# Optimization experiments

Measured on AMD Instinct MI355X. Metric: run time of the kernel, lower is better.

Reference implementation:

```python
import jax, jax.numpy as jnp
import numpy as np

B, S, D = 2, 2048, 512   # batch, seq_len, input_dim
H, E = 8, 512            # num_heads, per-head output_dim (full D per head, per source)
NEG = -1e9


def setup_inputs() -> dict:
    key = jax.random.key(0)
    ks = jax.random.split(key, 12)
    sc = 1.0 / np.sqrt(D)
    inp = {
        "query": jax.random.normal(ks[0], (B, S, D), jnp.float32),
        "key":   jax.random.normal(ks[1], (B, S, D), jnp.float32),
        "value": jax.random.normal(ks[2], (B, S, D), jnp.float32),
        "mask":  jax.random.randint(ks[3], (B, S, S), 0, 2).astype(bool),
        # stacked per-head Linear weights: [H, D, E] (x @ W layout)
        "Wq": jax.random.normal(ks[4], (H, D, E), jnp.float32) * sc,
        "bq": jax.random.normal(ks[5], (H, E), jnp.float32) * 0.02,
        "Wk": jax.random.normal(ks[6], (H, D, E), jnp.float32) * sc,
        "bk": jax.random.normal(ks[7], (H, E), jnp.float32) * 0.02,
        "Wv": jax.random.normal(ks[8], (H, D, E), jnp.float32) * sc,
        "bv": jax.random.normal(ks[9], (H, E), jnp.float32) * 0.02,
        # output projection: Linear(H*E, E)
        "Wo": jax.random.normal(ks[10], (H * E, E), jnp.float32) * (1.0 / np.sqrt(H * E)),
        "bo": jax.random.normal(ks[11], (E,), jnp.float32) * 0.02,
    }
    return inp


def reference(query, key, value, mask, Wq, bq, Wk, bk, Wv, bv, Wo, bo):
    # Batched per-head projections (replaces the Python per-head loop)
    q = jnp.einsum("bsd,hde->bhse", query, Wq) + bq[None, :, None, :]
    k = jnp.einsum("bsd,hde->bhse", key,   Wk) + bk[None, :, None, :]
    v = jnp.einsum("bsd,hde->bhse", value, Wv) + bv[None, :, None, :]
    # NOTE: source has NO 1/sqrt(d) scaling — kept faithful.
    scores = jnp.einsum("bhse,bhte->bhst", q, k)           # [B,H,S,S]
    scores = jnp.where(mask[:, None, :, :], scores, NEG)    # masked_fill(mask==0, -1e9)
    attn = jax.nn.softmax(scores, axis=-1)
    out = jnp.einsum("bhst,bhte->bhse", attn, v)            # [B,H,S,E]
    # concat heads along last dim in head order -> [B,S,H*E]
    cat = out.transpose(0, 2, 1, 3).reshape(out.shape[0], out.shape[2], -1)
    return cat @ Wo + bo
```

## Files before the change

### kernel.cpp

```cpp
#include <hip/hip_runtime.h>

#define B_  2
#define S_  2048
#define D_  512
#define H_  8
#define E_  512
#define HE_ 4096

typedef _Float16 half8_t  __attribute__((ext_vector_type(8)));
typedef _Float16 half4_t  __attribute__((ext_vector_type(4)));
typedef float    floatx4  __attribute__((ext_vector_type(4)));
typedef __attribute__((address_space(1))) const unsigned int* gas_ptr;
typedef __attribute__((address_space(3))) unsigned int*       las_ptr;

__global__ __launch_bounds__(256) void cast3_f16_kernel(
    const float* __restrict__ s0, const float* __restrict__ s1, const float* __restrict__ s2,
    _Float16* __restrict__ d0, _Float16* __restrict__ d1, _Float16* __restrict__ d2, int n4) {
    int i = blockIdx.x * 256 + threadIdx.x;
    if (i >= n4) return;
    const float* s = (blockIdx.y == 0) ? s0 : (blockIdx.y == 1) ? s1 : s2;
    _Float16*    d = (blockIdx.y == 0) ? d0 : (blockIdx.y == 1) ? d1 : d2;
    float4 v = ((const float4*)s)[i];
    half4_t h = { (_Float16)v.x, (_Float16)v.y, (_Float16)v.z, (_Float16)v.w };
    ((half4_t*)d)[i] = h;
}

__global__ __launch_bounds__(256) void transpose3_cast_kernel(
    const float* __restrict__ p0, const float* __restrict__ p1, const float* __restrict__ p2,
    _Float16* __restrict__ q0, _Float16* __restrict__ q1, _Float16* __restrict__ q2,
    int R, int C) {
    __shared__ float t[32][33];
    int which = blockIdx.z >> 3, hh = blockIdx.z & 7;
    const float* src = ((which == 0) ? p0 : (which == 1) ? p1 : p2) + (long long)hh * R * C;
    _Float16*    dst = ((which == 0) ? q0 : (which == 1) ? q1 : q2) + (long long)hh * R * C;
    int c0 = blockIdx.x * 32, r0 = blockIdx.y * 32;
    int tx = threadIdx.x, ty = threadIdx.y;
#pragma unroll
    for (int i = 0; i < 32; i += 8)
        t[ty + i][tx] = src[(long long)(r0 + ty + i) * C + (c0 + tx)];
    __syncthreads();
#pragma unroll
    for (int i = 0; i < 32; i += 8)
        dst[(long long)(c0 + ty + i) * R + (r0 + tx)] = (_Float16)t[tx][ty + i];
}

__global__ __launch_bounds__(256) void transpose_cast_kernel(const float* __restrict__ src,
                                                             _Float16* __restrict__ dst,
                                                             int R, int C) {
    __shared__ float t[32][33];
    int c0 = blockIdx.x * 32, r0 = blockIdx.y * 32;
    int tx = threadIdx.x, ty = threadIdx.y;
#pragma unroll
    for (int i = 0; i < 32; i += 8)
        t[ty + i][tx] = src[(long long)(r0 + ty + i) * C + (c0 + tx)];
    __syncthreads();
#pragma unroll
    for (int i = 0; i < 32; i += 8)
        dst[(long long)(c0 + ty + i) * R + (r0 + tx)] = (_Float16)t[tx][ty + i];
}


__device__ __forceinline__ void xcd_decode(int& z, int& by, int& bx) {
    int gx = gridDim.x, gy = gridDim.y, gz = gridDim.z;
    int bpz = gx * gy;
    int fid = blockIdx.x + gx * (blockIdx.y + gy * blockIdx.z);
    if ((gz & 7) == 0) {
        int xcd = fid & 7, sl = fid >> 3;
        int zg = gz >> 3;
        z = xcd * zg + sl / bpz;
        int inner = sl % bpz;
        by = inner / gx;
        bx = inner % gx;
    } else {
        z = blockIdx.z; by = blockIdx.y; bx = blockIdx.x;
    }
}

__global__ __launch_bounds__(256) void gemm_qkv_kernel(
    const _Float16* __restrict__ Xq, const _Float16* __restrict__ Xk, const _Float16* __restrict__ Xv,
    const _Float16* __restrict__ WqT, const _Float16* __restrict__ WkT, const _Float16* __restrict__ WvT,
    const float* __restrict__ bq, const float* __restrict__ bk, const float* __restrict__ bv,
    _Float16* __restrict__ Qb, _Float16* __restrict__ Kb, _Float16* __restrict__ VT)
{
    int z, byy, bxx;
    xcd_decode(z, byy, bxx);
    int which = z >> 4, zz = z & 15;
    int bb = zz >> 3, hh = zz & 7;
    const _Float16* A  = ((which == 0) ? Xq : (which == 1) ? Xk : Xv) + (long long)bb * S_ * D_;
    const _Float16* Bt = ((which == 0) ? WqT : (which == 1) ? WkT : WvT) + (long long)hh * E_ * D_;
    const float* bias  = ((which == 0) ? bq : (which == 1) ? bk : bv) + hh * E_;

    int m0 = byy * 128;
    int n0 = bxx * 128;

    __shared__ __align__(16) _Float16 As[2][128][32];
    __shared__ __align__(16) _Float16 Bs[2][128][32];

    int tid  = threadIdx.x;
    int wave = tid >> 6, lane = tid & 63;
    int quad = lane >> 4, l16 = lane & 15;
    int wy = (wave >> 1) * 64, wx = (wave & 1) * 64;
    int pw = wave & 1, rw = (wave >> 1) * 64;
    int sr = lane >> 2;
    int scg = ((lane & 3) ^ ((lane >> 3) & 3)) * 8;
    _Float16* lA0 = &As[pw][rw][0];
    _Float16* lB0 = &Bs[pw][rw][0];
    int cra = (quad ^ ((l16 >> 1) & 3)) * 8;

    floatx4 acc[4][4] = {};

    for (int k0 = 0; k0 < D_; k0 += 64) {
        if (k0) __syncthreads();
        const _Float16* gA = A + (long long)(m0 + rw + sr) * D_ + k0 + pw * 32 + scg;
        const _Float16* gB = Bt + (long long)(n0 + rw + sr) * D_ + k0 + pw * 32 + scg;
#pragma unroll
        for (int j = 0; j < 4; j++) {
            __builtin_amdgcn_global_load_lds((gas_ptr)(gA + (long long)(j * 16) * D_),
                                             (las_ptr)(lA0 + j * 512), 16, 0, 0);
            __builtin_amdgcn_global_load_lds((gas_ptr)(gB + (long long)(j * 16) * D_),
                                             (las_ptr)(lB0 + j * 512), 16, 0, 0);
        }
        __syncthreads();
#pragma unroll
        for (int kc = 0; kc < 2; kc++) {
            half8_t af[4], bf[4];
#pragma unroll
            for (int i = 0; i < 4; i++) {
                af[i] = *(const half8_t*)&As[kc][wy + i * 16 + l16][cra];
                bf[i] = *(const half8_t*)&Bs[kc][wx + i * 16 + l16][cra];
            }
#pragma unroll
            for (int mi = 0; mi < 4; mi++)
#pragma unroll
                for (int ni = 0; ni < 4; ni++)
                    acc[mi][ni] = __builtin_amdgcn_mfma_f32_16x16x32_f16(af[mi], bf[ni], acc[mi][ni], 0, 0, 0);
        }
    }

    if (which < 2) {
        _Float16* C = ((which == 0) ? Qb : Kb) + ((long long)(bb * H_ + hh)) * S_ * E_;
#pragma unroll
        for (int mi = 0; mi < 4; mi++)
#pragma unroll
            for (int ni = 0; ni < 4; ni++)
#pragma unroll
                for (int r = 0; r < 4; r++) {
                    int row = m0 + wy + mi * 16 + quad * 4 + r;
                    int col = n0 + wx + ni * 16 + l16;
                    C[(long long)row * E_ + col] = (_Float16)(acc[mi][ni][r] + bias[col]);
                }
    } else {
        _Float16* C = VT + ((long long)(bb * H_ + hh)) * E_ * S_;
#pragma unroll
        for (int mi = 0; mi < 4; mi++)
#pragma unroll
            for (int ni = 0; ni < 4; ni++) {
                int row = m0 + wy + mi * 16 + quad * 4;
                int col = n0 + wx + ni * 16 + l16;
                float bcol = bias[col];
                half4_t h4 = { (_Float16)(acc[mi][ni][0] + bcol), (_Float16)(acc[mi][ni][1] + bcol),
                               (_Float16)(acc[mi][ni][2] + bcol), (_Float16)(acc[mi][ni][3] + bcol) };
                *(half4_t*)(C + (long long)col * S_ + row) = h4;
            }
    }
}

__global__ __launch_bounds__(512, 2) void gemm_bt256_kernel(
    const _Float16* __restrict__ A, const _Float16* __restrict__ Bt,
    _Float16* __restrict__ C,
    int K, int lda, int ldb,
    long long a_z, long long b_z, long long c_b, long long c_h, int c_rs, int hdiv)
{
    int z, byy, bxx;
    xcd_decode(z, byy, bxx);
    int bb = z / hdiv, hh = z % hdiv;
    A  += (long long)z * a_z;
    Bt += (long long)z * b_z;
    _Float16* Cz = C + bb * c_b + hh * c_h;

    int m0 = byy * 256;
    int n0 = bxx * 256;

    __shared__ __align__(16) _Float16 As[4][256][32];
    __shared__ __align__(16) _Float16 Bs[4][256][32];

    int tid  = threadIdx.x;
    int wave = tid >> 6, lane = tid & 63;
    int quad = lane >> 4, l16 = lane & 15;
    int wm128 = (wave >> 2) * 128;
    int wn64  = (wave & 3) * 64;
    int wave16 = wave * 16;
    int sr = lane >> 2;
    int scg = ((lane & 3) ^ ((lane >> 3) & 3)) * 8;
    int cra = (quad ^ ((l16 >> 1) & 3)) * 8;

    auto STAGE = [&](int t) {
        int buf = t & 3;
        int kk = t << 5;
        const _Float16* gA = A + (long long)(m0 + wave16 + sr) * lda + kk + scg;
        const _Float16* gB = Bt + (long long)(n0 + wave16 + sr) * ldb + kk + scg;
        _Float16* lA = &As[buf][wave16][0];
        _Float16* lB = &Bs[buf][wave16][0];
#pragma unroll
        for (int j = 0; j < 2; j++) {
            __builtin_amdgcn_global_load_lds((gas_ptr)(gA + (long long)(j * 128) * lda),
                                             (las_ptr)(lA + j * 128 * 32), 16, 0, 0);
            __builtin_amdgcn_global_load_lds((gas_ptr)(gB + (long long)(j * 128) * ldb),
                                             (las_ptr)(lB + j * 128 * 32), 16, 0, 0);
        }
    };

    int nt = K >> 5;

    STAGE(0);
    if (nt > 1) STAGE(1);
    if (nt > 2) STAGE(2);
    if (nt > 2)      asm volatile("s_waitcnt vmcnt(8)" ::: "memory");
    else if (nt > 1) asm volatile("s_waitcnt vmcnt(4)" ::: "memory");
    else             asm volatile("s_waitcnt vmcnt(0)" ::: "memory");
    __builtin_amdgcn_s_barrier();

    floatx4 acc[8][4] = {};

    for (int t = 0; t < nt; ++t) {
        if (t + 3 < nt) STAGE(t + 3);
        int buf = t & 3;
        half8_t af[8], bf[4];
#pragma unroll
        for (int i = 0; i < 8; i++)
            af[i] = *(const half8_t*)&As[buf][wm128 + i * 16 + l16][cra];
#pragma unroll
        for (int i = 0; i < 4; i++)
            bf[i] = *(const half8_t*)&Bs[buf][wn64 + i * 16 + l16][cra];
#pragma unroll
        for (int mi = 0; mi < 8; mi++)
#pragma unroll
            for (int ni = 0; ni < 4; ni++)
                acc[mi][ni] = __builtin_amdgcn_mfma_f32_16x16x32_f16(af[mi], bf[ni], acc[mi][ni], 0, 0, 0);
        if (t + 1 < nt) {
            if (t + 3 < nt)      asm volatile("s_waitcnt vmcnt(8) lgkmcnt(0)" ::: "memory");
            else if (t + 2 < nt) asm volatile("s_waitcnt vmcnt(4) lgkmcnt(0)" ::: "memory");
            else                 asm volatile("s_waitcnt vmcnt(0) lgkmcnt(0)" ::: "memory");
            __builtin_amdgcn_s_barrier();
        }
    }

#pragma unroll
    for (int mi = 0; mi < 8; mi++)
#pragma unroll
        for (int ni = 0; ni < 4; ni++)
#pragma unroll
            for (int r = 0; r < 4; r++) {
                int row = m0 + wm128 + mi * 16 + quad * 4 + r;
                int col = n0 + wn64 + ni * 16 + l16;
                Cz[(long long)row * c_rs + col] = (_Float16)acc[mi][ni][r];
            }
}

__global__ __launch_bounds__(512) void softmax_mask8_kernel(_Float16* __restrict__ sc,
                                                            const int* __restrict__ mask)
{
    int b = blockIdx.z, s = blockIdx.x;
    int wave = threadIdx.x >> 6, lane = threadIdx.x & 63;
    _Float16* row = sc + ((long long)(b * H_ + wave) * S_ + s) * S_;
    const int* mrow = mask + ((long long)b * S_ + s) * S_;

    half8_t h[4];
    float v[32];
    float mx = -3.0e38f;
#pragma unroll
    for (int j = 0; j < 4; j++) {
        int c = j * 512 + lane * 8;
        h[j] = *(const half8_t*)(row + c);
        int4 mA = *(const int4*)(mrow + c);
        int4 mB = *(const int4*)(mrow + c + 4);
        int mm[8] = { mA.x, mA.y, mA.z, mA.w, mB.x, mB.y, mB.z, mB.w };
#pragma unroll
        for (int e = 0; e < 8; e++) {
            float val = mm[e] ? (float)h[j][e] : -1.0e9f;
            v[j * 8 + e] = val;
            mx = fmaxf(mx, val);
        }
    }
#pragma unroll
    for (int o = 32; o > 0; o >>= 1) mx = fmaxf(mx, __shfl_xor(mx, o));

    float sum = 0.0f;
#pragma unroll
    for (int i = 0; i < 32; i++) { v[i] = __expf(v[i] - mx); sum += v[i]; }
#pragma unroll
    for (int o = 32; o > 0; o >>= 1) sum += __shfl_xor(sum, o);

    float inv = 1.0f / sum;
#pragma unroll
    for (int j = 0; j < 4; j++) {
#pragma unroll
        for (int e = 0; e < 8; e++) h[j][e] = (_Float16)(v[j * 8 + e] * inv);
        *(half8_t*)(row + j * 512 + lane * 8) = h[j];
    }
}

__global__ __launch_bounds__(256) void gemm_bt_n64_splitk_kernel(
    const _Float16* __restrict__ A, const _Float16* __restrict__ Bt,
    const float* __restrict__ bias, float* __restrict__ C,
    int K, int lda, int ldb, int ldc, int ksplit)
{
    int m0 = blockIdx.y * 128;
    int n0 = blockIdx.x * 64;
    int kchunk = K / ksplit;
    int kbeg = blockIdx.z * kchunk;
    int kend = kbeg + kchunk;

    __shared__ __align__(16) _Float16 As[128][32];
    __shared__ __align__(16) _Float16 Bs[64][32];

    int tid  = threadIdx.x;
    int wave = tid >> 6, lane = tid & 63;
    int quad = lane >> 4, l16 = lane & 15;
    int wy = (wave >> 1) * 64, wx = (wave & 1) * 32;

    int srow = (wave << 4) + (lane >> 2);
    int scg = ((lane & 3) ^ ((lane >> 3) & 3)) * 8;
    _Float16* lA0 = &As[0][0] + (wave << 9);
    _Float16* lB0 = &Bs[0][0] + (wave << 9);
    int cra = (quad ^ ((l16 >> 1) & 3)) * 8;

    floatx4 acc[4][2] = {};

    for (int k0 = kbeg; k0 < kend; k0 += 32) {
        if (k0 != kbeg) __syncthreads();
        const _Float16* gA = A + (long long)(m0 + srow) * lda + k0 + scg;
        const _Float16* gB = Bt + (long long)(n0 + srow) * ldb + k0 + scg;
#pragma unroll
        for (int j = 0; j < 2; j++)
            __builtin_amdgcn_global_load_lds((gas_ptr)(gA + (long long)(j << 6) * lda),
                                             (las_ptr)(lA0 + (j << 11)), 16, 0, 0);
        __builtin_amdgcn_global_load_lds((gas_ptr)gB, (las_ptr)lB0, 16, 0, 0);
        __syncthreads();

        half8_t af[4], bf[2];
#pragma unroll
        for (int i = 0; i < 4; i++)
            af[i] = *(const half8_t*)&As[wy + i * 16 + l16][cra];
#pragma unroll
        for (int i = 0; i < 2; i++)
            bf[i] = *(const half8_t*)&Bs[wx + i * 16 + l16][cra];
#pragma unroll
        for (int mi = 0; mi < 4; mi++)
#pragma unroll
            for (int ni = 0; ni < 2; ni++)
                acc[mi][ni] = __builtin_amdgcn_mfma_f32_16x16x32_f16(af[mi], bf[ni], acc[mi][ni], 0, 0, 0);
    }

    int addb = (blockIdx.z == 0) && bias;
#pragma unroll
    for (int mi = 0; mi < 4; mi++)
#pragma unroll
        for (int ni = 0; ni < 2; ni++)
#pragma unroll
            for (int r = 0; r < 4; r++) {
                int row = m0 + wy + mi * 16 + quad * 4 + r;
                int col = n0 + wx + ni * 16 + l16;
                float v = acc[mi][ni][r];
                if (addb) v += bias[col];
                atomicAdd(&C[(long long)row * ldc + col], v);
            }
}

extern "C" void kernel_launch(void* const* d_in, const int* in_sizes, int n_in,
                              void* d_out, int out_size, void* d_ws, size_t ws_size,
                              hipStream_t stream)
{
    const float* qin = (const float*)d_in[0];
    const float* kin = (const float*)d_in[1];
    const float* vin = (const float*)d_in[2];
    const int*   mask = (const int*)d_in[3];
    const float* Wq = (const float*)d_in[4];
    const float* bq = (const float*)d_in[5];
    const float* Wk = (const float*)d_in[6];
    const float* bk = (const float*)d_in[7];
    const float* Wv = (const float*)d_in[8];
    const float* bv = (const float*)d_in[9];
    const float* Wo = (const float*)d_in[10];
    const float* bo = (const float*)d_in[11];
    float* out = (float*)d_out;

    char* ws = (char*)d_ws;
    size_t off = 0;
    _Float16* WoT = (_Float16*)(ws + off); off += (size_t)E_ * HE_ * 2;
    _Float16* Qb  = (_Float16*)(ws + off); off += (size_t)B_ * H_ * S_ * E_ * 2;
    _Float16* Kb  = (_Float16*)(ws + off); off += (size_t)B_ * H_ * S_ * E_ * 2;
    _Float16* VT  = (_Float16*)(ws + off); off += (size_t)B_ * H_ * E_ * S_ * 2;
    size_t region = off;
    _Float16* Xq  = (_Float16*)(ws + region);
    _Float16* Xk  = Xq  + (size_t)B_ * S_ * D_;
    _Float16* Xv  = Xk  + (size_t)B_ * S_ * D_;
    _Float16* WqT = Xv  + (size_t)B_ * S_ * D_;
    _Float16* WkT = WqT + (size_t)H_ * E_ * D_;
    _Float16* WvT = WkT + (size_t)H_ * E_ * D_;
    _Float16* SC  = (_Float16*)(ws + region);
    _Float16* cat = Qb;

    long long SE = (long long)S_ * E_;
    long long SS = (long long)S_ * S_;
    long long ES = (long long)E_ * S_;

    (void)hipMemsetAsync(d_out, 0, (size_t)out_size * sizeof(float), stream);

    int n4 = B_ * S_ * D_ / 4;
    cast3_f16_kernel<<<dim3(n4 / 256, 3), 256, 0, stream>>>(qin, kin, vin, Xq, Xk, Xv, n4);

    dim3 tb(32, 8);
    transpose3_cast_kernel<<<dim3(E_ / 32, D_ / 32, 24), tb, 0, stream>>>(
        Wq, Wk, Wv, WqT, WkT, WvT, D_, E_);
    transpose_cast_kernel<<<dim3(E_ / 32, HE_ / 32, 1), tb, 0, stream>>>(Wo, WoT, HE_, E_);

    gemm_qkv_kernel<<<dim3(E_ / 128, S_ / 128, 48), 256, 0, stream>>>(
        Xq, Xk, Xv, WqT, WkT, WvT, bq, bk, bv, Qb, Kb, VT);

    gemm_bt256_kernel<<<dim3(S_ / 256, S_ / 256, B_ * H_), 512, 0, stream>>>(
        Qb, Kb, SC, E_, E_, E_, SE, SE, 0, SS, S_, 32 );

    softmax_mask8_kernel<<<dim3(S_, 1, B_), 512, 0, stream>>>(SC, mask);

    gemm_bt256_kernel<<<dim3(E_ / 256, S_ / 256, B_ * H_), 512, 0, stream>>>(
        SC, VT, cat, S_, S_, S_, SS, ES, (long long)S_ * HE_, E_, HE_, H_);

    gemm_bt_n64_splitk_kernel<<<dim3(E_ / 64, (B_ * S_) / 128, 4), 256, 0, stream>>>(
        cat, WoT, bo, out, HE_, HE_, HE_, E_, 4);
}
```

Before: 533.3 us.

## Double-buffer LDS fragment reads in GEMM core and move QKV projection to 256 tiles

Factors the 256x256 GEMM main loop into a shared core that prefetches the next k-step's LDS fragments into a second register set while MFMAs run on the current one. MFMA sections get raised wave priority, and the barrier and waitcnt logic is restructured. The QKV projection moves from a 128x128 tile kernel onto this 256x256 core with 512 threads. The aim is to hide LDS read latency and raise per-block reuse, at the cost of more registers for the double fragments and fewer blocks in the QKV grid.

```diff
diff --git a/kernel.cpp b/kernel.cpp
--- a/kernel.cpp
+++ b/kernel.cpp
@@ -58,7 +58,6 @@
     for (int i = 0; i < 32; i += 8)
         dst[(long long)(c0 + ty + i) * R + (r0 + tx)] = (_Float16)t[tx][ty + i];
 }
-
 
 __device__ __forceinline__ void xcd_decode(int& z, int& by, int& bx) {
     int gx = gridDim.x, gy = gridDim.y, gz = gridDim.z;
@@ -76,114 +75,12 @@
     }
 }
 
-__global__ __launch_bounds__(256) void gemm_qkv_kernel(
-    const _Float16* __restrict__ Xq, const _Float16* __restrict__ Xk, const _Float16* __restrict__ Xv,
-    const _Float16* __restrict__ WqT, const _Float16* __restrict__ WkT, const _Float16* __restrict__ WvT,
-    const float* __restrict__ bq, const float* __restrict__ bk, const float* __restrict__ bv,
-    _Float16* __restrict__ Qb, _Float16* __restrict__ Kb, _Float16* __restrict__ VT)
-{
-    int z, byy, bxx;
-    xcd_decode(z, byy, bxx);
-    int which = z >> 4, zz = z & 15;
-    int bb = zz >> 3, hh = zz & 7;
-    const _Float16* A  = ((which == 0) ? Xq : (which == 1) ? Xk : Xv) + (long long)bb * S_ * D_;
-    const _Float16* Bt = ((which == 0) ? WqT : (which == 1) ? WkT : WvT) + (long long)hh * E_ * D_;
-    const float* bias  = ((which == 0) ? bq : (which == 1) ? bk : bv) + hh * E_;
-
-    int m0 = byy * 128;
-    int n0 = bxx * 128;
-
-    __shared__ __align__(16) _Float16 As[2][128][32];
-    __shared__ __align__(16) _Float16 Bs[2][128][32];
-
-    int tid  = threadIdx.x;
-    int wave = tid >> 6, lane = tid & 63;
-    int quad = lane >> 4, l16 = lane & 15;
-    int wy = (wave >> 1) * 64, wx = (wave & 1) * 64;
-    int pw = wave & 1, rw = (wave >> 1) * 64;
-    int sr = lane >> 2;
-    int scg = ((lane & 3) ^ ((lane >> 3) & 3)) * 8;
-    _Float16* lA0 = &As[pw][rw][0];
-    _Float16* lB0 = &Bs[pw][rw][0];
-    int cra = (quad ^ ((l16 >> 1) & 3)) * 8;
-
-    floatx4 acc[4][4] = {};
-
-    for (int k0 = 0; k0 < D_; k0 += 64) {
-        if (k0) __syncthreads();
-        const _Float16* gA = A + (long long)(m0 + rw + sr) * D_ + k0 + pw * 32 + scg;
-        const _Float16* gB = Bt + (long long)(n0 + rw + sr) * D_ + k0 + pw * 32 + scg;
-#pragma unroll
-        for (int j = 0; j < 4; j++) {
-            __builtin_amdgcn_global_load_lds((gas_ptr)(gA + (long long)(j * 16) * D_),
-                                             (las_ptr)(lA0 + j * 512), 16, 0, 0);
-            __builtin_amdgcn_global_load_lds((gas_ptr)(gB + (long long)(j * 16) * D_),
-                                             (las_ptr)(lB0 + j * 512), 16, 0, 0);
-        }
-        __syncthreads();
-#pragma unroll
-        for (int kc = 0; kc < 2; kc++) {
-            half8_t af[4], bf[4];
-#pragma unroll
-            for (int i = 0; i < 4; i++) {
-                af[i] = *(const half8_t*)&As[kc][wy + i * 16 + l16][cra];
-                bf[i] = *(const half8_t*)&Bs[kc][wx + i * 16 + l16][cra];
-            }
-#pragma unroll
-            for (int mi = 0; mi < 4; mi++)
-#pragma unroll
-                for (int ni = 0; ni < 4; ni++)
-                    acc[mi][ni] = __builtin_amdgcn_mfma_f32_16x16x32_f16(af[mi], bf[ni], acc[mi][ni], 0, 0, 0);
-        }
-    }
-
-    if (which < 2) {
-        _Float16* C = ((which == 0) ? Qb : Kb) + ((long long)(bb * H_ + hh)) * S_ * E_;
-#pragma unroll
-        for (int mi = 0; mi < 4; mi++)
-#pragma unroll
-            for (int ni = 0; ni < 4; ni++)
-#pragma unroll
-                for (int r = 0; r < 4; r++) {
-                    int row = m0 + wy + mi * 16 + quad * 4 + r;
-                    int col = n0 + wx + ni * 16 + l16;
-                    C[(long long)row * E_ + col] = (_Float16)(acc[mi][ni][r] + bias[col]);
-                }
-    } else {
-        _Float16* C = VT + ((long long)(bb * H_ + hh)) * E_ * S_;
-#pragma unroll
-        for (int mi = 0; mi < 4; mi++)
-#pragma unroll
-            for (int ni = 0; ni < 4; ni++) {
-                int row = m0 + wy + mi * 16 + quad * 4;
-                int col = n0 + wx + ni * 16 + l16;
-                float bcol = bias[col];
-                half4_t h4 = { (_Float16)(acc[mi][ni][0] + bcol), (_Float16)(acc[mi][ni][1] + bcol),
-                               (_Float16)(acc[mi][ni][2] + bcol), (_Float16)(acc[mi][ni][3] + bcol) };
-                *(half4_t*)(C + (long long)col * S_ + row) = h4;
-            }
-    }
-}
-
-__global__ __launch_bounds__(512, 2) void gemm_bt256_kernel(
+__device__ __forceinline__ void bt256_core(
     const _Float16* __restrict__ A, const _Float16* __restrict__ Bt,
-    _Float16* __restrict__ C,
-    int K, int lda, int ldb,
-    long long a_z, long long b_z, long long c_b, long long c_h, int c_rs, int hdiv)
-{
-    int z, byy, bxx;
-    xcd_decode(z, byy, bxx);
-    int bb = z / hdiv, hh = z % hdiv;
-    A  += (long long)z * a_z;
-    Bt += (long long)z * b_z;
-    _Float16* Cz = C + bb * c_b + hh * c_h;
-
-    int m0 = byy * 256;
-    int n0 = bxx * 256;
-
-    __shared__ __align__(16) _Float16 As[4][256][32];
-    __shared__ __align__(16) _Float16 Bs[4][256][32];
-
+    int lda, int ldb, int nt, int m0, int n0,
+    _Float16 (*As)[256][32], _Float16 (*Bs)[256][32],
+    floatx4 (&acc)[8][4])
+{
     int tid  = threadIdx.x;
     int wave = tid >> 6, lane = tid & 63;
     int quad = lane >> 4, l16 = lane & 15;
@@ -194,11 +91,13 @@
     int scg = ((lane & 3) ^ ((lane >> 3) & 3)) * 8;
     int cra = (quad ^ ((l16 >> 1) & 3)) * 8;
 
+    const _Float16* gA0 = A + (long long)(m0 + wave16 + sr) * lda + scg;
+    const _Float16* gB0 = Bt + (long long)(n0 + wave16 + sr) * ldb + scg;
+
     auto STAGE = [&](int t) {
         int buf = t & 3;
-        int kk = t << 5;
-        const _Float16* gA = A + (long long)(m0 + wave16 + sr) * lda + kk + scg;
-        const _Float16* gB = Bt + (long long)(n0 + wave16 + sr) * ldb + kk + scg;
+        const _Float16* gA = gA0 + (t << 5);
+        const _Float16* gB = gB0 + (t << 5);
         _Float16* lA = &As[buf][wave16][0];
         _Float16* lB = &Bs[buf][wave16][0];
 #pragma unroll
@@ -209,42 +108,85 @@
                                              (las_ptr)(lB + j * 128 * 32), 16, 0, 0);
         }
     };
-
-    int nt = K >> 5;
-
-    STAGE(0);
-    if (nt > 1) STAGE(1);
-    if (nt > 2) STAGE(2);
-    if (nt > 2)      asm volatile("s_waitcnt vmcnt(8)" ::: "memory");
-    else if (nt > 1) asm volatile("s_waitcnt vmcnt(4)" ::: "memory");
-    else             asm volatile("s_waitcnt vmcnt(0)" ::: "memory");
-    __builtin_amdgcn_s_barrier();
-
-    floatx4 acc[8][4] = {};
-
-    for (int t = 0; t < nt; ++t) {
-        if (t + 3 < nt) STAGE(t + 3);
+    auto DSREAD = [&](int t, half8_t (&fa)[8], half8_t (&fb)[4]) {
         int buf = t & 3;
-        half8_t af[8], bf[4];
 #pragma unroll
         for (int i = 0; i < 8; i++)
-            af[i] = *(const half8_t*)&As[buf][wm128 + i * 16 + l16][cra];
+            fa[i] = *(const half8_t*)&As[buf][wm128 + i * 16 + l16][cra];
 #pragma unroll
         for (int i = 0; i < 4; i++)
-            bf[i] = *(const half8_t*)&Bs[buf][wn64 + i * 16 + l16][cra];
+            fb[i] = *(const half8_t*)&Bs[buf][wn64 + i * 16 + l16][cra];
+    };
+    auto MFMA = [&](half8_t (&fa)[8], half8_t (&fb)[4]) {
+        __builtin_amdgcn_s_setprio(1);
 #pragma unroll
         for (int mi = 0; mi < 8; mi++)
 #pragma unroll
             for (int ni = 0; ni < 4; ni++)
-                acc[mi][ni] = __builtin_amdgcn_mfma_f32_16x16x32_f16(af[mi], bf[ni], acc[mi][ni], 0, 0, 0);
-        if (t + 1 < nt) {
-            if (t + 3 < nt)      asm volatile("s_waitcnt vmcnt(8) lgkmcnt(0)" ::: "memory");
-            else if (t + 2 < nt) asm volatile("s_waitcnt vmcnt(4) lgkmcnt(0)" ::: "memory");
-            else                 asm volatile("s_waitcnt vmcnt(0) lgkmcnt(0)" ::: "memory");
+                acc[mi][ni] = __builtin_amdgcn_mfma_f32_16x16x32_f16(fa[mi], fb[ni], acc[mi][ni], 0, 0, 0);
+        __builtin_amdgcn_s_setprio(0);
+    };
+    auto BODY = [&](int t, half8_t (&ca)[8], half8_t (&cb)[4],
+                    half8_t (&na)[8], half8_t (&nb)[4]) {
+        if (t + 3 < nt) {
+            STAGE(t + 3);
+            asm volatile("s_waitcnt vmcnt(8)" ::: "memory");
+            __builtin_amdgcn_s_barrier();
+        } else if (t + 3 == nt) {
+            asm volatile("s_waitcnt vmcnt(4)" ::: "memory");
+            __builtin_amdgcn_s_barrier();
+        } else if (t + 2 == nt) {
+            asm volatile("s_waitcnt vmcnt(0)" ::: "memory");
             __builtin_amdgcn_s_barrier();
         }
-    }
-
+        if (t + 1 < nt) DSREAD(t + 1, na, nb);
+        MFMA(ca, cb);
+        asm volatile("s_waitcnt lgkmcnt(0)" ::: "memory");
+        __builtin_amdgcn_sched_barrier(0);
+    };
+
+    half8_t fa0[8], fb0[4], fa1[8], fb1[4];
+
+    STAGE(0); STAGE(1); STAGE(2);
+    asm volatile("s_waitcnt vmcnt(8)" ::: "memory");
+    __builtin_amdgcn_s_barrier();
+    DSREAD(0, fa0, fb0);
+    asm volatile("s_waitcnt lgkmcnt(0)" ::: "memory");
+    __builtin_amdgcn_sched_barrier(0);
+
+    for (int t0 = 0; t0 < nt; t0 += 2) {
+        BODY(t0,     fa0, fb0, fa1, fb1);
+        BODY(t0 + 1, fa1, fb1, fa0, fb0);
+    }
+}
+
+__global__ __launch_bounds__(512, 2) void gemm_bt256_kernel(
+    const _Float16* __restrict__ A, const _Float16* __restrict__ Bt,
+    _Float16* __restrict__ C,
+    int K, int lda, int ldb,
+    long long a_z, long long b_z, long long c_b, long long c_h, int c_rs, int hdiv)
+{
+    int z, byy, bxx;
+    xcd_decode(z, byy, bxx);
+    int bb = z / hdiv, hh = z % hdiv;
+    A  += (long long)z * a_z;
+    Bt += (long long)z * b_z;
+    _Float16* Cz = C + bb * c_b + hh * c_h;
+
+    int m0 = byy * 256;
+    int n0 = bxx * 256;
+
+    __shared__ __align__(16) _Float16 As[4][256][32];
+    __shared__ __align__(16) _Float16 Bs[4][256][32];
+
+    floatx4 acc[8][4] = {};
+    bt256_core(A, Bt, lda, ldb, K >> 5, m0, n0, As, Bs, acc);
+
+    int tid  = threadIdx.x;
+    int wave = tid >> 6, lane = tid & 63;
+    int quad = lane >> 4, l16 = lane & 15;
+    int wm128 = (wave >> 2) * 128;
+    int wn64  = (wave & 3) * 64;
 #pragma unroll
     for (int mi = 0; mi < 8; mi++)
 #pragma unroll
@@ -255,6 +197,63 @@
                 int col = n0 + wn64 + ni * 16 + l16;
                 Cz[(long long)row * c_rs + col] = (_Float16)acc[mi][ni][r];
             }
+}
+
+__global__ __launch_bounds__(512, 2) void gemm_qkv256_kernel(
+    const _Float16* __restrict__ Xq, const _Float16* __restrict__ Xk, const _Float16* __restrict__ Xv,
+    const _Float16* __restrict__ WqT, const _Float16* __restrict__ WkT, const _Float16* __restrict__ WvT,
+    const float* __restrict__ bq, const float* __restrict__ bk, const float* __restrict__ bv,
+    _Float16* __restrict__ Qb, _Float16* __restrict__ Kb, _Float16* __restrict__ VT)
+{
+    int z, byy, bxx;
+    xcd_decode(z, byy, bxx);
+    int which = z >> 4, zz = z & 15;
+    int bb = zz >> 3, hh = zz & 7;
+    const _Float16* A  = ((which == 0) ? Xq : (which == 1) ? Xk : Xv) + (long long)bb * S_ * D_;
+    const _Float16* Bt = ((which == 0) ? WqT : (which == 1) ? WkT : WvT) + (long long)hh * E_ * D_;
+    const float* bias  = ((which == 0) ? bq : (which == 1) ? bk : bv) + hh * E_;
+
+    int m0 = byy * 256;
+    int n0 = bxx * 256;
+
+    __shared__ __align__(16) _Float16 As[4][256][32];
+    __shared__ __align__(16) _Float16 Bs[4][256][32];
+
+    floatx4 acc[8][4] = {};
+    bt256_core(A, Bt, D_, D_, D_ / 32, m0, n0, As, Bs, acc);
+
+    int tid  = threadIdx.x;
+    int wave = tid >> 6, lane = tid & 63;
+    int quad = lane >> 4, l16 = lane & 15;
+    int wm128 = (wave >> 2) * 128;
+    int wn64  = (wave & 3) * 64;
+
+    if (which < 2) {
+        _Float16* C = ((which == 0) ? Qb : Kb) + ((long long)(bb * H_ + hh)) * S_ * E_;
+#pragma unroll
+        for (int mi = 0; mi < 8; mi++)
+#pragma unroll
+            for (int ni = 0; ni < 4; ni++)
+#pragma unroll
+                for (int r = 0; r < 4; r++) {
+                    int row = m0 + wm128 + mi * 16 + quad * 4 + r;
+                    int col = n0 + wn64 + ni * 16 + l16;
+                    C[(long long)row * E_ + col] = (_Float16)(acc[mi][ni][r] + bias[col]);
+                }
+    } else {
+        _Float16* C = VT + ((long long)(bb * H_ + hh)) * E_ * S_;
+#pragma unroll
+        for (int mi = 0; mi < 8; mi++)
+#pragma unroll
+            for (int ni = 0; ni < 4; ni++) {
+                int row = m0 + wm128 + mi * 16 + quad * 4;
+                int col = n0 + wn64 + ni * 16 + l16;
+                float bcol = bias[col];
+                half4_t h4 = { (_Float16)(acc[mi][ni][0] + bcol), (_Float16)(acc[mi][ni][1] + bcol),
+                               (_Float16)(acc[mi][ni][2] + bcol), (_Float16)(acc[mi][ni][3] + bcol) };
+                *(half4_t*)(C + (long long)col * S_ + row) = h4;
+            }
+    }
 }
 
 __global__ __launch_bounds__(512) void softmax_mask8_kernel(_Float16* __restrict__ sc,
@@ -415,7 +414,7 @@
         Wq, Wk, Wv, WqT, WkT, WvT, D_, E_);
     transpose_cast_kernel<<<dim3(E_ / 32, HE_ / 32, 1), tb, 0, stream>>>(Wo, WoT, HE_, E_);
 
-    gemm_qkv_kernel<<<dim3(E_ / 128, S_ / 128, 48), 256, 0, stream>>>(
+    gemm_qkv256_kernel<<<dim3(E_ / 256, S_ / 256, 48), 512, 0, stream>>>(
         Xq, Xk, Xv, WqT, WkT, WvT, bq, bk, bv, Qb, Kb, VT);
 
     gemm_bt256_kernel<<<dim3(S_ / 256, S_ / 256, B_ * H_), 512, 0, stream>>>(
```

After: 519.0 us. 2.7% less time.
